# Optimization experiments

Hardware: AMD Instinct MI355X
Metric: run time of the kernel (lower is better)

## Reference

```python
import jax, jax.numpy as jnp
import numpy as np

B, T, E, H, R = 1, 2048, 4096, 16, 64
D = E // H
SCALE_ATTN = float(np.sqrt(D))


def _i8_linear(x, W, b, alpha, beta):
    # W8A8B8O8Linear: int8 in, int8 weight/bias, int8 out with requant epilogue
    acc = jnp.einsum('bte,oe->bto', x.astype(jnp.int32), W.astype(jnp.int32)).astype(jnp.float32)
    y = alpha * acc + beta * b.astype(jnp.float32)
    return jnp.clip(jnp.round(y), -128, 127).astype(jnp.int8)


def _rotate_every_two(x):
    x1, x2 = x[..., ::2], x[..., 1::2]
    return jnp.stack([-x2, x1], axis=-1).reshape(x.shape)


def _sincos(seq_len, dim):
    inv_freq = 1.0 / (10000.0 ** (jnp.arange(0, dim, 2, dtype=jnp.float32) / dim))
    ang = jnp.arange(seq_len, dtype=jnp.float32)[:, None] * inv_freq[None, :]
    return jnp.sin(ang), jnp.cos(ang)


def _apply_rotary(x, sin, cos):
    # duplicate_interleave -> repeat each freq twice along last dim
    sin = jnp.repeat(sin, 2, axis=-1)[None, :, None, :]
    cos = jnp.repeat(cos, 2, axis=-1)[None, :, None, :]
    return x * cos + _rotate_every_two(x) * sin


def setup_inputs():
    key = jax.random.key(0)
    ks = jax.random.split(key, 9)
    i8 = lambda k, s: jax.random.randint(k, s, -128, 128, dtype=jnp.int32).astype(jnp.int8)
    return {
        'hidden_states': i8(ks[0], (B, T, E)),
        'Wq': i8(ks[1], (E, E)), 'bq': i8(ks[2], (E,)),
        'Wk': i8(ks[3], (E, E)), 'bk': i8(ks[4], (E,)),
        'Wv': i8(ks[5], (E, E)), 'bv': i8(ks[6], (E,)),
        'Wo': i8(ks[7], (E, E)),
        'b_out': jax.random.normal(ks[8], (E,), dtype=jnp.float32),
        'alpha_q': 2e-4, 'beta_q': 1.0,
        'alpha_k': 2e-4, 'beta_k': 1.0,
        'alpha_v': 2e-4, 'beta_v': 1.0,
        'alpha_qk': 1e-3, 'alpha_pv': 1e-2, 'alpha_out': 2e-4,
    }


def reference(hidden_states, Wq, bq, Wk, bk, Wv, bv, Wo, b_out,
              alpha_q, beta_q, alpha_k, beta_k, alpha_v, beta_v,
              alpha_qk, alpha_pv, alpha_out):
    # int8 q/k/v projections -> [B, T, H, D]
    q = _i8_linear(hidden_states, Wq, bq, alpha_q, beta_q).reshape(B, T, H, D)
    k = _i8_linear(hidden_states, Wk, bk, alpha_k, beta_k).reshape(B, T, H, D)
    v = _i8_linear(hidden_states, Wv, bv, alpha_v, beta_v).reshape(B, T, H, D)
    v = v.transpose(0, 2, 1, 3)  # [B, H, T, D] int8

    # fused rotary on first R dims (float math on dequantized-per-tensor int8 codes)
    sin, cos = _sincos(T, R)
    qf, kf = q.astype(jnp.float32), k.astype(jnp.float32)
    qf = jnp.concatenate([_apply_rotary(qf[..., :R], sin, cos), qf[..., R:]], axis=-1)
    kf = jnp.concatenate([_apply_rotary(kf[..., :R], sin, cos), kf[..., R:]], axis=-1)
    # torch .to(int8) truncates toward zero
    to_i8 = lambda x: jnp.clip(jnp.trunc(x), -128, 127).astype(jnp.int8)
    q = to_i8(qf.transpose(0, 2, 1, 3))  # [B, H, T, D]
    k = to_i8(kf.transpose(0, 2, 1, 3))

    scores = alpha_qk * jnp.einsum('bhtd,bhsd->bhts', q.astype(jnp.int32), k.astype(jnp.int32)).astype(jnp.float32)
    causal = jnp.tril(jnp.ones((T, T), dtype=bool))
    scores = jnp.where(causal, scores, jnp.finfo(jnp.float32).min)
    probs = jax.nn.softmax(scores / SCALE_ATTN, axis=-1)
    probs = jnp.round(probs * 127.0).astype(jnp.int8)  # requant probs to int8

    acc = jnp.einsum('bhts,bhsd->bhtd', probs.astype(jnp.int32), v.astype(jnp.int32)).astype(jnp.float32)
    attn_out = jnp.clip(jnp.round(alpha_pv * acc), -128, 127).astype(jnp.int8)
    attn_out = attn_out.transpose(0, 2, 1, 3).reshape(B, T, E)  # merge heads

    # W8A8BFP32OFP32Linear
    out = alpha_out * jnp.einsum('bte,oe->bto', attn_out.astype(jnp.int32), Wo.astype(jnp.int32)).astype(jnp.float32) + b_out
    return out
```

## Files before the change

### kernel.cpp

```cpp
#include <hip/hip_runtime.h>
#include <cstdint>
#include <cmath>

#define T_ 2048
#define E_ 4096
#define H_ 16
#define D_ 256
#define NF 32

typedef int v4i  __attribute__((ext_vector_type(4)));

__device__ __forceinline__ int dot4(int a, int b, int c) {
#if __has_builtin(__builtin_amdgcn_sdot4)
  return __builtin_amdgcn_sdot4(a, b, c, false);
#else
  c += ((a << 24) >> 24) * ((b << 24) >> 24);
  c += ((a << 16) >> 24) * ((b << 16) >> 24);
  c += ((a <<  8) >> 24) * ((b <<  8) >> 24);
  c += (a >> 24) * (b >> 24);
  return c;
#endif
}

__device__ __forceinline__ int pack4i(int4 v) {
  return (v.x & 255) | ((v.y & 255) << 8) | ((v.z & 255) << 16) | (v.w << 24);
}

#define GLD_LDS16(g, l)                                                        \
  __builtin_amdgcn_global_load_lds(                                            \
      (const __attribute__((address_space(1))) void*)(g),                      \
      (__attribute__((address_space(3))) void*)(l), 16, 0, 0)

__global__ void sincos_kernel(float* __restrict__ sinT, float* __restrict__ cosT) {
  int idx = blockIdx.x * 256 + threadIdx.x;
  int t = idx >> 5, j = idx & 31;
  float invf = (float)exp(-(double)j * (log(10000.0) / 32.0));
  float ang = (float)t * invf;
  sinT[idx] = (float)sin((double)ang);
  cosT[idx] = (float)cos((double)ang);
}

__global__ __launch_bounds__(256) void repack_kernel(const int* __restrict__ src,
                                                     int8_t* __restrict__ dst) {
  size_t i = (size_t)blockIdx.x * 256 + threadIdx.x;
  const int4* s = (const int4*)src + i * 4;
  int4 a = s[0], b = s[1], c = s[2], d = s[3];
  int4 o;
  o.x = pack4i(a); o.y = pack4i(b); o.z = pack4i(c); o.w = pack4i(d);
  ((int4*)dst)[i] = o;
}

__global__ __launch_bounds__(256) void qkv_gemm_mfma(
    const int8_t* __restrict__ x8,
    const int8_t* __restrict__ Wq8, const int* __restrict__ bq,
    const int8_t* __restrict__ Wk8, const int* __restrict__ bk,
    const int8_t* __restrict__ Wv8, const int* __restrict__ bv,
    const float* __restrict__ alpq, const float* __restrict__ betq,
    const float* __restrict__ alpk, const float* __restrict__ betk,
    const float* __restrict__ alpv, const float* __restrict__ betv,
    int8_t* __restrict__ Q8, int8_t* __restrict__ K8, int8_t* __restrict__ VT)
{
  const int mode = blockIdx.z;
  const int8_t* __restrict__ W = (mode == 0) ? Wq8 : (mode == 1 ? Wk8 : Wv8);
  const int* __restrict__ bs   = (mode == 0) ? bq  : (mode == 1 ? bk  : bv);
  const float alpha = (mode == 0) ? alpq[0] : (mode == 1 ? alpk[0] : alpv[0]);
  const float beta  = (mode == 0) ? betq[0] : (mode == 1 ? betk[0] : betv[0]);

  __shared__ int8_t As[128 * 64];
  __shared__ int8_t Bs[128 * 64];

  const int tid  = threadIdx.x;
  const int wave = tid >> 6, lane = tid & 63;
  const int wm = wave >> 1, wn = wave & 1;
  const int t0 = blockIdx.x * 128, o0 = blockIdx.y * 128;

  const int srow = lane >> 2;
  const int scol = (lane & 3) * 16;
  const int col  = lane & 15;
  const int quad = lane >> 4;

  v4i acc[4][4] = {};

  const int8_t* gA0 = x8 + (size_t)(t0 + wave * 32 + srow) * E_ + scol;
  const int8_t* gB0 = W  + (size_t)(o0 + wave * 32 + srow) * E_ + scol;

  for (int e0 = 0; e0 < E_; e0 += 64) {
    __syncthreads();
    GLD_LDS16(gA0 + e0,                 As + wave * 2048);
    GLD_LDS16(gA0 + e0 + 16 * E_,       As + wave * 2048 + 1024);
    GLD_LDS16(gB0 + e0,                 Bs + wave * 2048);
    GLD_LDS16(gB0 + e0 + 16 * E_,       Bs + wave * 2048 + 1024);
    __syncthreads();

    v4i a[4], b[4];
    #pragma unroll
    for (int i = 0; i < 4; ++i)
      a[i] = *(const v4i*)(As + (wm * 64 + i * 16 + col) * 64 + quad * 16);
    #pragma unroll
    for (int j = 0; j < 4; ++j)
      b[j] = *(const v4i*)(Bs + (wn * 64 + j * 16 + col) * 64 + quad * 16);
    #pragma unroll
    for (int i = 0; i < 4; ++i)
      #pragma unroll
      for (int j = 0; j < 4; ++j)
        acc[i][j] = __builtin_amdgcn_mfma_i32_16x16x64_i8(a[i], b[j], acc[i][j], 0, 0, 0);
  }

  int8_t* __restrict__ dst = (mode == 0) ? Q8 : (mode == 1 ? K8 : VT);
  #pragma unroll
  for (int j = 0; j < 4; ++j) {
    const int o  = o0 + wn * 64 + j * 16 + col;
    const int h  = o >> 8;
    const int dd = o & 255;
    const float bb = (float)bs[o];
    #pragma unroll
    for (int i = 0; i < 4; ++i) {
      const int tb = t0 + wm * 64 + i * 16 + quad * 4;
      int qb[4];
      #pragma unroll
      for (int r = 0; r < 4; ++r) {
        float v = __fadd_rn(__fmul_rn(alpha, (float)acc[i][j][r]),
                            __fmul_rn(beta, bb));
        v = rintf(v);
        v = fminf(fmaxf(v, -128.0f), 127.0f);
        qb[r] = (int)v;
      }
      if (mode == 2) {
        int packed = (qb[0] & 255) | ((qb[1] & 255) << 8) |
                     ((qb[2] & 255) << 16) | ((qb[3] & 255) << 24);
        *(int*)(dst + ((size_t)h * 256 + dd) * T_ + tb) = packed;
      } else {
        #pragma unroll
        for (int r = 0; r < 4; ++r)
          dst[((size_t)h * T_ + tb + r) * D_ + dd] = (int8_t)qb[r];
      }
    }
  }
}

__global__ __launch_bounds__(256) void rope_kernel(
    int8_t* __restrict__ Q8, int8_t* __restrict__ K8,
    const float* __restrict__ sinT, const float* __restrict__ cosT)
{
  int idx = blockIdx.x * 256 + threadIdx.x;
  int c = idx & 3;
  int t = (idx >> 2) & (T_ - 1);
  int h = (idx >> 13) & (H_ - 1);
  int m = idx >> 17;
  int8_t* base = (m == 0 ? Q8 : K8) + ((size_t)h * T_ + t) * D_ + c * 16;
  int4 v = *(int4*)base;
  int u[4] = {v.x, v.y, v.z, v.w};
  const int jb = c * 8;
  #pragma unroll
  for (int ui = 0; ui < 4; ++ui) {
    const int j = jb + ui * 2;
    const float s0 = sinT[t * NF + j],     c0 = cosT[t * NF + j];
    const float s1 = sinT[t * NF + j + 1], c1 = cosT[t * NF + j + 1];
    const int w = u[ui];
    float y0 = (float)((w << 24) >> 24);
    float y1 = (float)((w << 16) >> 24);
    float y2 = (float)((w <<  8) >> 24);
    float y3 = (float)(w >> 24);
    float r0 = __fadd_rn(__fmul_rn(y0, c0), __fmul_rn(-y1, s0));
    float r1 = __fadd_rn(__fmul_rn(y1, c0), __fmul_rn( y0, s0));
    float r2 = __fadd_rn(__fmul_rn(y2, c1), __fmul_rn(-y3, s1));
    float r3 = __fadd_rn(__fmul_rn(y3, c1), __fmul_rn( y2, s1));
    int q0 = (int)fminf(fmaxf(truncf(r0), -128.0f), 127.0f);
    int q1 = (int)fminf(fmaxf(truncf(r1), -128.0f), 127.0f);
    int q2 = (int)fminf(fmaxf(truncf(r2), -128.0f), 127.0f);
    int q3 = (int)fminf(fmaxf(truncf(r3), -128.0f), 127.0f);
    u[ui] = (q0 & 255) | ((q1 & 255) << 8) | ((q2 & 255) << 16) | ((q3 & 255) << 24);
  }
  int4 ov; ov.x = u[0]; ov.y = u[1]; ov.z = u[2]; ov.w = u[3];
  *(int4*)base = ov;
}

__global__ __launch_bounds__(256) void out_gemm_mfma(
    const int8_t* __restrict__ xa, const int8_t* __restrict__ Wo8,
    const float* __restrict__ b_out, const float* __restrict__ p_aout,
    float* __restrict__ out)
{
  const float alpha = p_aout[0];
  __shared__ int8_t As[128 * 64];
  __shared__ int8_t Bs[128 * 64];

  const int tid  = threadIdx.x;
  const int wave = tid >> 6, lane = tid & 63;
  const int wm = wave >> 1, wn = wave & 1;
  const int t0 = blockIdx.x * 128, o0 = blockIdx.y * 128;
  const int srow = lane >> 2, scol = (lane & 3) * 16;
  const int col = lane & 15, quad = lane >> 4;

  v4i acc[4][4] = {};
  const int8_t* gA0 = xa  + (size_t)(t0 + wave * 32 + srow) * E_ + scol;
  const int8_t* gB0 = Wo8 + (size_t)(o0 + wave * 32 + srow) * E_ + scol;

  for (int e0 = 0; e0 < E_; e0 += 64) {
    __syncthreads();
    GLD_LDS16(gA0 + e0,            As + wave * 2048);
    GLD_LDS16(gA0 + e0 + 16 * E_,  As + wave * 2048 + 1024);
    GLD_LDS16(gB0 + e0,            Bs + wave * 2048);
    GLD_LDS16(gB0 + e0 + 16 * E_,  Bs + wave * 2048 + 1024);
    __syncthreads();

    v4i a[4], b[4];
    #pragma unroll
    for (int i = 0; i < 4; ++i)
      a[i] = *(const v4i*)(As + (wm * 64 + i * 16 + col) * 64 + quad * 16);
    #pragma unroll
    for (int j = 0; j < 4; ++j)
      b[j] = *(const v4i*)(Bs + (wn * 64 + j * 16 + col) * 64 + quad * 16);
    #pragma unroll
    for (int i = 0; i < 4; ++i)
      #pragma unroll
      for (int j = 0; j < 4; ++j)
        acc[i][j] = __builtin_amdgcn_mfma_i32_16x16x64_i8(a[i], b[j], acc[i][j], 0, 0, 0);
  }

  #pragma unroll
  for (int j = 0; j < 4; ++j) {
    const int o = o0 + wn * 64 + j * 16 + col;
    const float bb = b_out[o];
    #pragma unroll
    for (int i = 0; i < 4; ++i) {
      #pragma unroll
      for (int r = 0; r < 4; ++r) {
        const int t = t0 + wm * 64 + i * 16 + quad * 4 + r;
        out[(size_t)t * E_ + o] = __fadd_rn(__fmul_rn(alpha, (float)acc[i][j][r]), bb);
      }
    }
  }
}

__global__ __launch_bounds__(256) void attn_ms_chunk(
    const int8_t* __restrict__ Q8, const int8_t* __restrict__ K8,
    const float* __restrict__ p_aqk,
    float* __restrict__ mPart, float* __restrict__ sPart)
{
  const int ch = blockIdx.x;
  const int qi = blockIdx.y;
  const int h  = blockIdx.z;
  if ((ch << 2) > qi) return;

  __shared__ int8_t Qs[4 * 4096];
  __shared__ int8_t KVs[16384];
  __shared__ float  mred[64][2];
  __shared__ float  sred[64][2];

  const int t0  = qi * 64;
  const int tid = threadIdx.x;
  const int wave = tid >> 6, lane = tid & 63;
  const int wm = wave >> 1, wn = wave & 1;
  const int col = lane & 15, quad = lane >> 4;
  const int srow = lane >> 2, scol = (lane & 3) * 16;
  const float aqk = p_aqk[0] * 0.0625f;

  {
    const int8_t* g = Q8 + ((size_t)h * T_ + t0 + wave * 16 + srow) * D_ + scol;
    #pragma unroll
    for (int c = 0; c < 4; ++c)
      GLD_LDS16(g + c * 64, Qs + c * 4096 + wave * 1024);
  }

  const int it0 = ch * 4;
  const int it1 = (it0 + 3 < qi) ? (it0 + 3) : qi;

  float m[8], sm[8];
  #pragma unroll
  for (int u = 0; u < 8; ++u) { m[u] = -INFINITY; sm[u] = 0.0f; }

  for (int it = it0; it <= it1; ++it) {
    const int s0 = it * 64;
    __syncthreads();
    {
      const int8_t* g = K8 + ((size_t)h * T_ + s0 + wave * 16 + srow) * D_ + scol;
      #pragma unroll
      for (int c = 0; c < 4; ++c)
        GLD_LDS16(g + c * 64, KVs + c * 4096 + wave * 1024);
    }
    __syncthreads();
    v4i accS[2][2] = {};
    #pragma unroll
    for (int c = 0; c < 4; ++c) {
      v4i a[2], b[2];
      #pragma unroll
      for (int i = 0; i < 2; ++i)
        a[i] = *(const v4i*)(Qs + c * 4096 + (wm * 32 + i * 16 + col) * 64 + quad * 16);
      #pragma unroll
      for (int j = 0; j < 2; ++j)
        b[j] = *(const v4i*)(KVs + c * 4096 + (wn * 32 + j * 16 + col) * 64 + quad * 16);
      #pragma unroll
      for (int i = 0; i < 2; ++i)
        #pragma unroll
        for (int j = 0; j < 2; ++j)
          accS[i][j] = __builtin_amdgcn_mfma_i32_16x16x64_i8(a[i], b[j], accS[i][j], 0, 0, 0);
    }
    const bool diag = (s0 == t0);
    #pragma unroll
    for (int i = 0; i < 2; ++i) {
      #pragma unroll
      for (int r = 0; r < 4; ++r) {
        const int ri = i * 4 + r;
        const int qrow = t0 + wm * 32 + i * 16 + quad * 4 + r;
        #pragma unroll
        for (int j = 0; j < 2; ++j) {
          const int s = s0 + wn * 32 + j * 16 + col;
          if (!diag || s <= qrow) {
            float l = __fmul_rn(aqk, (float)accS[i][j][r]);
            if (l > m[ri]) { sm[ri] = sm[ri] * expf(m[ri] - l) + 1.0f; m[ri] = l; }
            else           { sm[ri] += expf(l - m[ri]); }
          }
        }
      }
    }
  }

  #pragma unroll
  for (int u = 0; u < 8; ++u) {
    #pragma unroll
    for (int off = 1; off < 16; off <<= 1) {
      float om = __shfl_xor(m[u], off);
      float os = __shfl_xor(sm[u], off);
      float mm = fmaxf(m[u], om);
      float e1 = (m[u] == mm) ? 1.0f : expf(m[u] - mm);
      float e2 = (om   == mm) ? 1.0f : expf(om - mm);
      sm[u] = sm[u] * e1 + os * e2;
      m[u] = mm;
    }
  }
  __syncthreads();
  if (col == 0) {
    #pragma unroll
    for (int u = 0; u < 8; ++u) {
      int row = wm * 32 + (u >> 2) * 16 + quad * 4 + (u & 3);
      mred[row][wn] = m[u];
      sred[row][wn] = sm[u];
    }
  }
  __syncthreads();
  if (col == 0 && wn == 0) {
    #pragma unroll
    for (int u = 0; u < 8; ++u) {
      int row = wm * 32 + (u >> 2) * 16 + quad * 4 + (u & 3);
      float m0 = mred[row][0], m1 = mred[row][1];
      float sa = sred[row][0], sb = sred[row][1];
      float mm = fmaxf(m0, m1);
      float e0 = (m0 == mm) ? 1.0f : expf(m0 - mm);
      float e1 = (m1 == mm) ? 1.0f : expf(m1 - mm);
      size_t base = (((size_t)h * 32 + qi) * 64 + row) * 8 + ch;
      mPart[base] = mm;
      sPart[base] = __fadd_rn(__fmul_rn(sa, e0), __fmul_rn(sb, e1));
    }
  }
}

__global__ __launch_bounds__(256) void attn_ms_combine(
    const float* __restrict__ mPart, const float* __restrict__ sPart,
    float* __restrict__ mFg, float* __restrict__ sFg)
{
  int idx = blockIdx.x * 256 + threadIdx.x;
  int t = idx & (T_ - 1), h = idx >> 11;
  int qi = t >> 6, row = t & 63;
  int nch = (qi >> 2) + 1;
  const float* mp = mPart + (((size_t)h * 32 + qi) * 64 + row) * 8;
  const float* sp = sPart + (((size_t)h * 32 + qi) * 64 + row) * 8;
  float m = mp[0], s = sp[0];
  for (int c = 1; c < nch; ++c) {
    float mc = mp[c], sc = sp[c];
    float mm = fmaxf(m, mc);
    float e1 = (m  == mm) ? 1.0f : expf(m - mm);
    float e2 = (mc == mm) ? 1.0f : expf(mc - mm);
    s = __fadd_rn(__fmul_rn(s, e1), __fmul_rn(sc, e2));
    m = mm;
  }
  mFg[idx] = m;
  sFg[idx] = s;
}

__global__ __launch_bounds__(256) void attn_pv_chunk(
    const int8_t* __restrict__ Q8, const int8_t* __restrict__ K8,
    const int8_t* __restrict__ VT,
    const float* __restrict__ p_aqk,
    const float* __restrict__ mFg, const float* __restrict__ sFg,
    int* __restrict__ P0, int* __restrict__ P1)
{
  const int cc = blockIdx.x;
  const int qi = 31 - blockIdx.y;
  const int h  = blockIdx.z;
  if (cc == 1 && qi < 16) return;

  __shared__ int8_t Qs[4 * 4096];
  __shared__ int8_t KVs[16384];
  __shared__ int8_t Ps[64][64];

  const int t0  = qi * 64;
  const int tid = threadIdx.x;
  const int wave = tid >> 6, lane = tid & 63;
  const int wm = wave >> 1, wn = wave & 1;
  const int col = lane & 15, quad = lane >> 4;
  const int srow = lane >> 2, scol = (lane & 3) * 16;
  const float aqk = p_aqk[0] * 0.0625f;

  {
    const int8_t* g = Q8 + ((size_t)h * T_ + t0 + wave * 16 + srow) * D_ + scol;
    #pragma unroll
    for (int c = 0; c < 4; ++c)
      GLD_LDS16(g + c * 64, Qs + c * 4096 + wave * 1024);
  }

  float mF[8], sF[8];
  #pragma unroll
  for (int u = 0; u < 8; ++u) {
    const int row = wm * 32 + (u >> 2) * 16 + quad * 4 + (u & 3);
    mF[u] = mFg[h * T_ + t0 + row];
    sF[u] = sFg[h * T_ + t0 + row];
  }

  const int it0 = cc * 16;
  const int it1 = (it0 + 15 < qi) ? (it0 + 15) : qi;

  v4i pv[2][8] = {};
  for (int it = it0; it <= it1; ++it) {
    const int s0 = it * 64;
    __syncthreads();
    {
      const int8_t* g = K8 + ((size_t)h * T_ + s0 + wave * 16 + srow) * D_ + scol;
      #pragma unroll
      for (int c = 0; c < 4; ++c)
        GLD_LDS16(g + c * 64, KVs + c * 4096 + wave * 1024);
    }
    __syncthreads();
    v4i accS[2][2] = {};
    #pragma unroll
    for (int c = 0; c < 4; ++c) {
      v4i a[2], b[2];
      #pragma unroll
      for (int i = 0; i < 2; ++i)
        a[i] = *(const v4i*)(Qs + c * 4096 + (wm * 32 + i * 16 + col) * 64 + quad * 16);
      #pragma unroll
      for (int j = 0; j < 2; ++j)
        b[j] = *(const v4i*)(KVs + c * 4096 + (wn * 32 + j * 16 + col) * 64 + quad * 16);
      #pragma unroll
      for (int i = 0; i < 2; ++i)
        #pragma unroll
        for (int j = 0; j < 2; ++j)
          accS[i][j] = __builtin_amdgcn_mfma_i32_16x16x64_i8(a[i], b[j], accS[i][j], 0, 0, 0);
    }
    __syncthreads();
    {
      #pragma unroll
      for (int c = 0; c < 4; ++c) {
        const int drow = (wave * 4 + c) * 16 + srow;
        GLD_LDS16(VT + ((size_t)h * 256 + drow) * T_ + s0 + scol,
                  KVs + (wave * 4 + c) * 1024);
      }
    }
    const bool diag = (s0 == t0);
    #pragma unroll
    for (int i = 0; i < 2; ++i) {
      #pragma unroll
      for (int r = 0; r < 4; ++r) {
        const int ri = i * 4 + r;
        const int qrow = t0 + wm * 32 + i * 16 + quad * 4 + r;
        #pragma unroll
        for (int j = 0; j < 2; ++j) {
          const int s = s0 + wn * 32 + j * 16 + col;
          int q = 0;
          if (!diag || s <= qrow) {
            float l = __fmul_rn(aqk, (float)accS[i][j][r]);
            float p = expf(l - mF[ri]) / sF[ri];
            q = (int)rintf(__fmul_rn(p, 127.0f));
          }
          Ps[wm * 32 + i * 16 + quad * 4 + r][wn * 32 + j * 16 + col] = (int8_t)q;
        }
      }
    }
    __syncthreads();
    v4i a2[2], b2[8];
    #pragma unroll
    for (int i = 0; i < 2; ++i)
      a2[i] = *(const v4i*)&Ps[wm * 32 + i * 16 + col][quad * 16];
    #pragma unroll
    for (int dt = 0; dt < 8; ++dt)
      b2[dt] = *(const v4i*)(KVs + (wn * 128 + dt * 16 + col) * 64 + quad * 16);
    #pragma unroll
    for (int i = 0; i < 2; ++i)
      #pragma unroll
      for (int dt = 0; dt < 8; ++dt)
        pv[i][dt] = __builtin_amdgcn_mfma_i32_16x16x64_i8(a2[i], b2[dt], pv[i][dt], 0, 0, 0);
  }

  int* __restrict__ dst = (cc == 0)
      ? P0 + (((size_t)h * 32 + qi) << 14)
      : P1 + (((size_t)h * 16 + (qi - 16)) << 14);
  #pragma unroll
  for (int i = 0; i < 2; ++i) {
    #pragma unroll
    for (int r = 0; r < 4; ++r) {
      const int trow = wm * 32 + i * 16 + quad * 4 + r;
      #pragma unroll
      for (int dt = 0; dt < 8; ++dt) {
        const int d = wn * 128 + dt * 16 + col;
        dst[trow * 256 + d] = pv[i][dt][r];
      }
    }
  }
}

__global__ __launch_bounds__(256) void attn_pv_combine(
    const int* __restrict__ P0, const int* __restrict__ P1,
    const float* __restrict__ p_apv, int8_t* __restrict__ attn8)
{
  const float apv = p_apv[0];
  int idx = blockIdx.x * 256 + threadIdx.x;
  int d4  = idx & 63;
  int row = (idx >> 6) & 63;
  int qi  = (idx >> 12) & 31;
  int h   = idx >> 17;
  size_t off = (((size_t)h * 32 + qi) << 14) + row * 256 + d4 * 4;
  int4 a = *(const int4*)(P0 + off);
  if (qi >= 16) {
    size_t off1 = (((size_t)h * 16 + (qi - 16)) << 14) + row * 256 + d4 * 4;
    int4 b1 = *(const int4*)(P1 + off1);
    a.x += b1.x; a.y += b1.y; a.z += b1.z; a.w += b1.w;
  }
  int q[4];
  int vv[4] = {a.x, a.y, a.z, a.w};
  #pragma unroll
  for (int r = 0; r < 4; ++r) {
    float y = rintf(__fmul_rn(apv, (float)vv[r]));
    y = fminf(fmaxf(y, -128.0f), 127.0f);
    q[r] = (int)y;
  }
  int packed = (q[0] & 255) | ((q[1] & 255) << 8) | ((q[2] & 255) << 16) | ((q[3] & 255) << 24);
  int t = qi * 64 + row;
  *(int*)(attn8 + (size_t)t * E_ + h * D_ + d4 * 4) = packed;
}

__global__ __launch_bounds__(256) void attn_mfma(
    const int8_t* __restrict__ Q8, const int8_t* __restrict__ K8,
    const int8_t* __restrict__ VT,
    const float* __restrict__ p_aqk, const float* __restrict__ p_apv,
    int8_t* __restrict__ attn8)
{
  __shared__ int8_t Qs[4 * 4096];
  __shared__ int8_t KVs[16384];
  __shared__ int8_t Ps[64][64];
  __shared__ float  mred[64][2];
  __shared__ float  sred[64][2];

  const int h   = blockIdx.y;
  const int t0  = blockIdx.x * 64;
  const int tid = threadIdx.x;
  const int wave = tid >> 6, lane = tid & 63;
  const int wm = wave >> 1, wn = wave & 1;
  const int col = lane & 15, quad = lane >> 4;
  const int srow = lane >> 2, scol = (lane & 3) * 16;
  const float aqk = p_aqk[0] * 0.0625f;
  const float apv = p_apv[0];

  {
    const int8_t* g = Q8 + ((size_t)h * T_ + t0 + wave * 16 + srow) * D_ + scol;
    #pragma unroll
    for (int c = 0; c < 4; ++c)
      GLD_LDS16(g + c * 64, Qs + c * 4096 + wave * 1024);
  }

  const int nt = t0 / 64 + 1;

  float m[8], sm[8];
  #pragma unroll
  for (int u = 0; u < 8; ++u) { m[u] = -INFINITY; sm[u] = 0.0f; }

  for (int it = 0; it < nt; ++it) {
    const int s0 = it * 64;
    __syncthreads();
    {
      const int8_t* g = K8 + ((size_t)h * T_ + s0 + wave * 16 + srow) * D_ + scol;
      #pragma unroll
      for (int c = 0; c < 4; ++c)
        GLD_LDS16(g + c * 64, KVs + c * 4096 + wave * 1024);
    }
    __syncthreads();
    v4i accS[2][2] = {};
    #pragma unroll
    for (int c = 0; c < 4; ++c) {
      v4i a[2], b[2];
      #pragma unroll
      for (int i = 0; i < 2; ++i)
        a[i] = *(const v4i*)(Qs + c * 4096 + (wm * 32 + i * 16 + col) * 64 + quad * 16);
      #pragma unroll
      for (int j = 0; j < 2; ++j)
        b[j] = *(const v4i*)(KVs + c * 4096 + (wn * 32 + j * 16 + col) * 64 + quad * 16);
      #pragma unroll
      for (int i = 0; i < 2; ++i)
        #pragma unroll
        for (int j = 0; j < 2; ++j)
          accS[i][j] = __builtin_amdgcn_mfma_i32_16x16x64_i8(a[i], b[j], accS[i][j], 0, 0, 0);
    }
    const bool diag = (s0 == t0);
    #pragma unroll
    for (int i = 0; i < 2; ++i) {
      #pragma unroll
      for (int r = 0; r < 4; ++r) {
        const int ri = i * 4 + r;
        const int qrow = t0 + wm * 32 + i * 16 + quad * 4 + r;
        #pragma unroll
        for (int j = 0; j < 2; ++j) {
          const int s = s0 + wn * 32 + j * 16 + col;
          if (!diag || s <= qrow) {
            float l = __fmul_rn(aqk, (float)accS[i][j][r]);
            if (l > m[ri]) { sm[ri] = sm[ri] * expf(m[ri] - l) + 1.0f; m[ri] = l; }
            else           { sm[ri] += expf(l - m[ri]); }
          }
        }
      }
    }
  }

  #pragma unroll
  for (int u = 0; u < 8; ++u) {
    #pragma unroll
    for (int off = 1; off < 16; off <<= 1) {
      float om = __shfl_xor(m[u], off);
      float os = __shfl_xor(sm[u], off);
      float mm = fmaxf(m[u], om);
      float e1 = (m[u] == mm) ? 1.0f : expf(m[u] - mm);
      float e2 = (om   == mm) ? 1.0f : expf(om - mm);
      sm[u] = sm[u] * e1 + os * e2;
      m[u] = mm;
    }
  }
  __syncthreads();
  if (col == 0) {
    #pragma unroll
    for (int u = 0; u < 8; ++u) {
      int row = wm * 32 + (u >> 2) * 16 + quad * 4 + (u & 3);
      mred[row][wn] = m[u];
      sred[row][wn] = sm[u];
    }
  }
  __syncthreads();
  float mF[8], sF[8];
  #pragma unroll
  for (int u = 0; u < 8; ++u) {
    int row = wm * 32 + (u >> 2) * 16 + quad * 4 + (u & 3);
    float m0 = mred[row][0], m1 = mred[row][1];
    float sa = sred[row][0], sb = sred[row][1];
    float mm = fmaxf(m0, m1);
    float e0 = (m0 == mm) ? 1.0f : expf(m0 - mm);
    float e1 = (m1 == mm) ? 1.0f : expf(m1 - mm);
    mF[u] = mm;
    sF[u] = __fadd_rn(__fmul_rn(sa, e0), __fmul_rn(sb, e1));
  }

  v4i pv[2][8] = {};
  for (int it = 0; it < nt; ++it) {
    const int s0 = it * 64;
    __syncthreads();
    {
      const int8_t* g = K8 + ((size_t)h * T_ + s0 + wave * 16 + srow) * D_ + scol;
      #pragma unroll
      for (int c = 0; c < 4; ++c)
        GLD_LDS16(g + c * 64, KVs + c * 4096 + wave * 1024);
    }
    __syncthreads();
    v4i accS[2][2] = {};
    #pragma unroll
    for (int c = 0; c < 4; ++c) {
      v4i a[2], b[2];
      #pragma unroll
      for (int i = 0; i < 2; ++i)
        a[i] = *(const v4i*)(Qs + c * 4096 + (wm * 32 + i * 16 + col) * 64 + quad * 16);
      #pragma unroll
      for (int j = 0; j < 2; ++j)
        b[j] = *(const v4i*)(KVs + c * 4096 + (wn * 32 + j * 16 + col) * 64 + quad * 16);
      #pragma unroll
      for (int i = 0; i < 2; ++i)
        #pragma unroll
        for (int j = 0; j < 2; ++j)
          accS[i][j] = __builtin_amdgcn_mfma_i32_16x16x64_i8(a[i], b[j], accS[i][j], 0, 0, 0);
    }
    __syncthreads();
    {
      #pragma unroll
      for (int c = 0; c < 4; ++c) {
        const int drow = (wave * 4 + c) * 16 + srow;
        GLD_LDS16(VT + ((size_t)h * 256 + drow) * T_ + s0 + scol,
                  KVs + (wave * 4 + c) * 1024);
      }
    }
    const bool diag = (s0 == t0);
    #pragma unroll
    for (int i = 0; i < 2; ++i) {
      #pragma unroll
      for (int r = 0; r < 4; ++r) {
        const int ri = i * 4 + r;
        const int qrow = t0 + wm * 32 + i * 16 + quad * 4 + r;
        #pragma unroll
        for (int j = 0; j < 2; ++j) {
          const int s = s0 + wn * 32 + j * 16 + col;
          int q = 0;
          if (!diag || s <= qrow) {
            float l = __fmul_rn(aqk, (float)accS[i][j][r]);
            float p = expf(l - mF[ri]) / sF[ri];
            q = (int)rintf(__fmul_rn(p, 127.0f));
          }
          Ps[wm * 32 + i * 16 + quad * 4 + r][wn * 32 + j * 16 + col] = (int8_t)q;
        }
      }
    }
    __syncthreads();
    v4i a2[2], b2[8];
    #pragma unroll
    for (int i = 0; i < 2; ++i)
      a2[i] = *(const v4i*)&Ps[wm * 32 + i * 16 + col][quad * 16];
    #pragma unroll
    for (int dt = 0; dt < 8; ++dt)
      b2[dt] = *(const v4i*)(KVs + (wn * 128 + dt * 16 + col) * 64 + quad * 16);
    #pragma unroll
    for (int i = 0; i < 2; ++i)
      #pragma unroll
      for (int dt = 0; dt < 8; ++dt)
        pv[i][dt] = __builtin_amdgcn_mfma_i32_16x16x64_i8(a2[i], b2[dt], pv[i][dt], 0, 0, 0);
  }

  #pragma unroll
  for (int i = 0; i < 2; ++i) {
    #pragma unroll
    for (int r = 0; r < 4; ++r) {
      const int t = t0 + wm * 32 + i * 16 + quad * 4 + r;
      #pragma unroll
      for (int dt = 0; dt < 8; ++dt) {
        const int d = wn * 128 + dt * 16 + col;
        float y = rintf(__fmul_rn(apv, (float)pv[i][dt][r]));
        y = fminf(fmaxf(y, -128.0f), 127.0f);
        attn8[(size_t)t * E_ + h * D_ + d] = (int8_t)(int)y;
      }
    }
  }
}

__global__ __launch_bounds__(256) void qkv_gemm_fb(
    const int* __restrict__ xp,
    const int* __restrict__ Wqp, const int* __restrict__ bq,
    const int* __restrict__ Wkp, const int* __restrict__ bk,
    const int* __restrict__ Wvp, const int* __restrict__ bv,
    const float* __restrict__ alpq, const float* __restrict__ betq,
    const float* __restrict__ alpk, const float* __restrict__ betk,
    const float* __restrict__ alpv, const float* __restrict__ betv,
    const float* __restrict__ sinT, const float* __restrict__ cosT,
    int8_t* __restrict__ Q8, int8_t* __restrict__ K8, int8_t* __restrict__ VT)
{
  const int mode = blockIdx.z;
  const int* __restrict__ Wp = (mode == 0) ? Wqp : (mode == 1 ? Wkp : Wvp);
  const int* __restrict__ bs = (mode == 0) ? bq  : (mode == 1 ? bk  : bv);
  const float alpha = (mode == 0) ? alpq[0] : (mode == 1 ? alpk[0] : alpv[0]);
  const float beta  = (mode == 0) ? betq[0] : (mode == 1 ? betk[0] : betv[0]);

  __shared__ int As[64 * 17];
  __shared__ int Bs[64 * 17];
  const int tid = threadIdx.x;
  const int tx = tid & 15, ty = tid >> 4;
  const int t0 = blockIdx.x * 64, o0 = blockIdx.y * 64;
  const int lrow = tid >> 2, lc = tid & 3;
  int acc[4][4] = {};

  for (int e0 = 0; e0 < E_; e0 += 64) {
    const int* xr = xp + (size_t)(t0 + lrow) * E_ + e0 + lc * 16;
    const int* wr = Wp + (size_t)(o0 + lrow) * E_ + e0 + lc * 16;
    int a4[4], b4[4];
    #pragma unroll
    for (int u = 0; u < 4; ++u) a4[u] = pack4i(((const int4*)xr)[u]);
    #pragma unroll
    for (int u = 0; u < 4; ++u) b4[u] = pack4i(((const int4*)wr)[u]);
    __syncthreads();
    int* ap = &As[lrow * 17 + lc * 4];
    ap[0] = a4[0]; ap[1] = a4[1]; ap[2] = a4[2]; ap[3] = a4[3];
    int* bp = &Bs[lrow * 17 + lc * 4];
    bp[0] = b4[0]; bp[1] = b4[1]; bp[2] = b4[2]; bp[3] = b4[3];
    __syncthreads();
    #pragma unroll
    for (int kk = 0; kk < 16; ++kk) {
      int a[4], b[4];
      #pragma unroll
      for (int i = 0; i < 4; ++i) a[i] = As[(ty * 4 + i) * 17 + kk];
      #pragma unroll
      for (int j = 0; j < 4; ++j) b[j] = Bs[(tx * 4 + j) * 17 + kk];
      #pragma unroll
      for (int i = 0; i < 4; ++i)
        #pragma unroll
        for (int j = 0; j < 4; ++j)
          acc[i][j] = dot4(a[i], b[j], acc[i][j]);
    }
  }

  const int ob = o0 + tx * 4;
  const int h  = ob >> 8;
  const int dd = ob & 255;
  #pragma unroll
  for (int i = 0; i < 4; ++i) {
    const int t = t0 + ty * 4 + i;
    float y[4];
    #pragma unroll
    for (int j = 0; j < 4; ++j) {
      float v = __fadd_rn(__fmul_rn(alpha, (float)acc[i][j]),
                          __fmul_rn(beta, (float)bs[ob + j]));
      v = rintf(v);
      y[j] = fminf(fmaxf(v, -128.0f), 127.0f);
    }
    int q0, q1, q2, q3;
    if (mode < 2 && dd < 64) {
      const int j0 = dd >> 1;
      const float s0 = sinT[t * NF + j0],     c0 = cosT[t * NF + j0];
      const float s1 = sinT[t * NF + j0 + 1], c1 = cosT[t * NF + j0 + 1];
      float r0 = __fadd_rn(__fmul_rn(y[0], c0), __fmul_rn(-y[1], s0));
      float r1 = __fadd_rn(__fmul_rn(y[1], c0), __fmul_rn( y[0], s0));
      float r2 = __fadd_rn(__fmul_rn(y[2], c1), __fmul_rn(-y[3], s1));
      float r3 = __fadd_rn(__fmul_rn(y[3], c1), __fmul_rn( y[2], s1));
      q0 = (int)fminf(fmaxf(truncf(r0), -128.0f), 127.0f);
      q1 = (int)fminf(fmaxf(truncf(r1), -128.0f), 127.0f);
      q2 = (int)fminf(fmaxf(truncf(r2), -128.0f), 127.0f);
      q3 = (int)fminf(fmaxf(truncf(r3), -128.0f), 127.0f);
    } else {
      q0 = (int)y[0]; q1 = (int)y[1]; q2 = (int)y[2]; q3 = (int)y[3];
    }
    if (mode == 2) {
      VT[((size_t)h * 256 + dd + 0) * T_ + t] = (int8_t)q0;
      VT[((size_t)h * 256 + dd + 1) * T_ + t] = (int8_t)q1;
      VT[((size_t)h * 256 + dd + 2) * T_ + t] = (int8_t)q2;
      VT[((size_t)h * 256 + dd + 3) * T_ + t] = (int8_t)q3;
    } else {
      int8_t* dst = (mode == 0) ? Q8 : K8;
      int packed = (q0 & 255) | ((q1 & 255) << 8) | ((q2 & 255) << 16) | ((q3 & 255) << 24);
      *(int*)(dst + ((size_t)h * T_ + t) * D_ + dd) = packed;
    }
  }
}

__global__ __launch_bounds__(256) void out_gemm_fb(
    const int8_t* __restrict__ xa, const int* __restrict__ Wop,
    const float* __restrict__ b_out, const float* __restrict__ p_aout,
    float* __restrict__ out)
{
  __shared__ int As[64 * 17];
  __shared__ int Bs[64 * 17];
  const float alpha = p_aout[0];
  const int tid = threadIdx.x;
  const int tx = tid & 15, ty = tid >> 4;
  const int t0 = blockIdx.x * 64, o0 = blockIdx.y * 64;
  const int lrow = tid >> 2, lc = tid & 3;
  int acc[4][4] = {};

  for (int e0 = 0; e0 < E_; e0 += 64) {
    int4 av4 = *(const int4*)(xa + (size_t)(t0 + lrow) * E_ + e0 + lc * 16);
    const int* wr = Wop + (size_t)(o0 + lrow) * E_ + e0 + lc * 16;
    int b4[4];
    #pragma unroll
    for (int u = 0; u < 4; ++u) b4[u] = pack4i(((const int4*)wr)[u]);
    __syncthreads();
    int* ap = &As[lrow * 17 + lc * 4];
    ap[0] = av4.x; ap[1] = av4.y; ap[2] = av4.z; ap[3] = av4.w;
    int* bp = &Bs[lrow * 17 + lc * 4];
    bp[0] = b4[0]; bp[1] = b4[1]; bp[2] = b4[2]; bp[3] = b4[3];
    __syncthreads();
    #pragma unroll
    for (int kk = 0; kk < 16; ++kk) {
      int a[4], b[4];
      #pragma unroll
      for (int i = 0; i < 4; ++i) a[i] = As[(ty * 4 + i) * 17 + kk];
      #pragma unroll
      for (int j = 0; j < 4; ++j) b[j] = Bs[(tx * 4 + j) * 17 + kk];
      #pragma unroll
      for (int i = 0; i < 4; ++i)
        #pragma unroll
        for (int j = 0; j < 4; ++j)
          acc[i][j] = dot4(a[i], b[j], acc[i][j]);
    }
  }
  #pragma unroll
  for (int i = 0; i < 4; ++i) {
    const int t = t0 + ty * 4 + i;
    const int ob = o0 + tx * 4;
    #pragma unroll
    for (int j = 0; j < 4; ++j) {
      out[(size_t)t * E_ + ob + j] =
          __fadd_rn(__fmul_rn(alpha, (float)acc[i][j]), b_out[ob + j]);
    }
  }
}

extern "C" void kernel_launch(void* const* d_in, const int* in_sizes, int n_in,
                              void* d_out, int out_size, void* d_ws, size_t ws_size,
                              hipStream_t stream) {
  const int* hs   = (const int*)d_in[0];
  const int* Wq   = (const int*)d_in[1];
  const int* bq   = (const int*)d_in[2];
  const int* Wk   = (const int*)d_in[3];
  const int* bk   = (const int*)d_in[4];
  const int* Wv   = (const int*)d_in[5];
  const int* bv   = (const int*)d_in[6];
  const int* Wo   = (const int*)d_in[7];
  const float* b_out = (const float*)d_in[8];
  const float* aq   = (const float*)d_in[9];
  const float* btq  = (const float*)d_in[10];
  const float* ak   = (const float*)d_in[11];
  const float* btk  = (const float*)d_in[12];
  const float* av   = (const float*)d_in[13];
  const float* btv  = (const float*)d_in[14];
  const float* aqk  = (const float*)d_in[15];
  const float* apv  = (const float*)d_in[16];
  const float* aout = (const float*)d_in[17];

  const size_t SEG = (size_t)H_ * T_ * D_;
  char* ws = (char*)d_ws;
  int8_t* Q8    = (int8_t*)ws;
  int8_t* K8    = Q8 + SEG;
  int8_t* VT    = K8 + SEG;
  int8_t* attn8 = VT + SEG;
  int8_t* x8    = attn8;
  float*  sinT  = (float*)(ws + 4 * SEG);
  float*  cosT  = sinT + T_ * NF;
  int8_t* Wq8   = (int8_t*)(cosT + T_ * NF);
  int8_t* Wk8   = Wq8 + (size_t)E_ * E_;
  int8_t* Wv8   = Wk8 + (size_t)E_ * E_;
  int8_t* Wo8   = Wv8 + (size_t)E_ * E_;
  const size_t NEED = 4 * SEG + 2 * (size_t)T_ * NF * 4 + 4 * (size_t)E_ * E_;
  const bool big = (ws_size >= NEED);

  sincos_kernel<<<(T_ * NF) / 256, 256, 0, stream>>>(sinT, cosT);

  if (big) {
    repack_kernel<<<(T_ * E_ / 16) / 256, 256, 0, stream>>>(hs, x8);
    repack_kernel<<<(E_ * E_ / 16) / 256, 256, 0, stream>>>(Wq, Wq8);
    repack_kernel<<<(E_ * E_ / 16) / 256, 256, 0, stream>>>(Wk, Wk8);
    repack_kernel<<<(E_ * E_ / 16) / 256, 256, 0, stream>>>(Wv, Wv8);
    repack_kernel<<<(E_ * E_ / 16) / 256, 256, 0, stream>>>(Wo, Wo8);
    qkv_gemm_mfma<<<dim3(T_ / 128, E_ / 128, 3), 256, 0, stream>>>(
        x8, Wq8, bq, Wk8, bk, Wv8, bv, aq, btq, ak, btk, av, btv, Q8, K8, VT);
    rope_kernel<<<(2 * H_ * T_ * 4) / 256, 256, 0, stream>>>(Q8, K8, sinT, cosT);

    int*   P1g   = (int*)Wq8;
    int*   P0g   = (int*)Wk8;
    float* mPart = (float*)attn8;
    float* sPart = mPart + (size_t)H_ * 32 * 64 * 8;
    float* mFg   = sPart + (size_t)H_ * 32 * 64 * 8;
    float* sFg   = mFg + (size_t)H_ * T_;

    attn_ms_chunk<<<dim3(8, 32, H_), 256, 0, stream>>>(Q8, K8, aqk, mPart, sPart);
    attn_ms_combine<<<(H_ * T_) / 256, 256, 0, stream>>>(mPart, sPart, mFg, sFg);
    attn_pv_chunk<<<dim3(2, 32, H_), 256, 0, stream>>>(
        Q8, K8, VT, aqk, mFg, sFg, P0g, P1g);
    attn_pv_combine<<<(H_ * 32 * 64 * 64) / 256, 256, 0, stream>>>(
        P0g, P1g, apv, attn8);

    out_gemm_mfma<<<dim3(T_ / 128, E_ / 128), 256, 0, stream>>>(
        attn8, Wo8, b_out, aout, (float*)d_out);
  } else {
    qkv_gemm_fb<<<dim3(T_ / 64, E_ / 64, 3), 256, 0, stream>>>(
        hs, Wq, bq, Wk, bk, Wv, bv, aq, btq, ak, btk, av, btv,
        sinT, cosT, Q8, K8, VT);
    attn_mfma<<<dim3(T_ / 64, H_), 256, 0, stream>>>(Q8, K8, VT, aqk, apv, attn8);
    out_gemm_fb<<<dim3(T_ / 64, E_ / 64), 256, 0, stream>>>(
        attn8, Wo, b_out, aout, (float*)d_out);
  }
}
```

Before: 701.3 us.

## Triple-buffer LDS with async prefetch and XOR swizzle in QKV/out GEMMs

Both int8 MFMA GEMMs (QKV projection and output projection) switch from a single LDS buffer guarded by two barriers per k-step to a 3-stage ring. Loads are issued two tiles ahead and gated with a vmcnt wait plus one barrier, so global-to-LDS traffic overlaps the MFMA work. The LDS layout also gets an XOR swizzle on the 16-byte column chunks to reduce bank conflicts on the fragment reads, and s_setprio raises wave priority around the MFMA burst. LDS use per block triples to 48KB, which may limit occupancy; the launch bounds now request 3 blocks per SM.

```diff
diff --git a/kernel.cpp b/kernel.cpp
--- a/kernel.cpp
+++ b/kernel.cpp
@@ -50,7 +50,7 @@
   ((int4*)dst)[i] = o;
 }
 
-__global__ __launch_bounds__(256) void qkv_gemm_mfma(
+__global__ __launch_bounds__(256, 3) void qkv_gemm_mfma(
     const int8_t* __restrict__ x8,
     const int8_t* __restrict__ Wq8, const int* __restrict__ bq,
     const int8_t* __restrict__ Wk8, const int* __restrict__ bk,
@@ -66,8 +66,8 @@
   const float alpha = (mode == 0) ? alpq[0] : (mode == 1 ? alpk[0] : alpv[0]);
   const float beta  = (mode == 0) ? betq[0] : (mode == 1 ? betk[0] : betv[0]);
 
-  __shared__ int8_t As[128 * 64];
-  __shared__ int8_t Bs[128 * 64];
+  __shared__ int8_t As[3][8192];
+  __shared__ int8_t Bs[3][8192];
 
   const int tid  = threadIdx.x;
   const int wave = tid >> 6, lane = tid & 63;
@@ -75,7 +75,7 @@
   const int t0 = blockIdx.x * 128, o0 = blockIdx.y * 128;
 
   const int srow = lane >> 2;
-  const int scol = (lane & 3) * 16;
+  const int scol = ((lane & 3) ^ ((lane >> 3) & 3)) * 16;
   const int col  = lane & 15;
   const int quad = lane >> 4;
 
@@ -84,27 +84,52 @@
   const int8_t* gA0 = x8 + (size_t)(t0 + wave * 32 + srow) * E_ + scol;
   const int8_t* gB0 = W  + (size_t)(o0 + wave * 32 + srow) * E_ + scol;
 
-  for (int e0 = 0; e0 < E_; e0 += 64) {
-    __syncthreads();
-    GLD_LDS16(gA0 + e0,                 As + wave * 2048);
-    GLD_LDS16(gA0 + e0 + 16 * E_,       As + wave * 2048 + 1024);
-    GLD_LDS16(gB0 + e0,                 Bs + wave * 2048);
-    GLD_LDS16(gB0 + e0 + 16 * E_,       Bs + wave * 2048 + 1024);
-    __syncthreads();
-
+#define STAGE_QKV(bufi, kt) do {                                               \
+    const int e0_ = (kt) * 64;                                                 \
+    GLD_LDS16(gA0 + e0_,           As[bufi] + wave * 2048);                    \
+    GLD_LDS16(gA0 + e0_ + 16 * E_, As[bufi] + wave * 2048 + 1024);             \
+    GLD_LDS16(gB0 + e0_,           Bs[bufi] + wave * 2048);                    \
+    GLD_LDS16(gB0 + e0_ + 16 * E_, Bs[bufi] + wave * 2048 + 1024);             \
+  } while (0)
+
+  int aoff[4], boff[4];
+  #pragma unroll
+  for (int i = 0; i < 4; ++i) {
+    const int ra = wm * 64 + i * 16 + col;
+    aoff[i] = ra * 64 + ((quad ^ ((ra >> 1) & 3)) * 16);
+    const int rb = wn * 64 + i * 16 + col;
+    boff[i] = rb * 64 + ((quad ^ ((rb >> 1) & 3)) * 16);
+  }
+
+  STAGE_QKV(0, 0);
+  STAGE_QKV(1, 1);
+
+  int cur = 0;
+  for (int kt = 0; kt < 64; ++kt) {
+    if (kt == 63) asm volatile("s_waitcnt vmcnt(0)" ::: "memory");
+    else          asm volatile("s_waitcnt vmcnt(4)" ::: "memory");
+    __builtin_amdgcn_s_barrier();
+    if (kt < 62) {
+      int nb = cur + 2; if (nb >= 3) nb -= 3;
+      STAGE_QKV(nb, kt + 2);
+    }
     v4i a[4], b[4];
     #pragma unroll
     for (int i = 0; i < 4; ++i)
-      a[i] = *(const v4i*)(As + (wm * 64 + i * 16 + col) * 64 + quad * 16);
+      a[i] = *(const v4i*)(As[cur] + aoff[i]);
     #pragma unroll
     for (int j = 0; j < 4; ++j)
-      b[j] = *(const v4i*)(Bs + (wn * 64 + j * 16 + col) * 64 + quad * 16);
+      b[j] = *(const v4i*)(Bs[cur] + boff[j]);
+    __builtin_amdgcn_s_setprio(1);
     #pragma unroll
     for (int i = 0; i < 4; ++i)
       #pragma unroll
       for (int j = 0; j < 4; ++j)
         acc[i][j] = __builtin_amdgcn_mfma_i32_16x16x64_i8(a[i], b[j], acc[i][j], 0, 0, 0);
-  }
+    __builtin_amdgcn_s_setprio(0);
+    cur = (cur == 2) ? 0 : cur + 1;
+  }
+#undef STAGE_QKV
 
   int8_t* __restrict__ dst = (mode == 0) ? Q8 : (mode == 1 ? K8 : VT);
   #pragma unroll
@@ -175,47 +200,73 @@
   *(int4*)base = ov;
 }
 
-__global__ __launch_bounds__(256) void out_gemm_mfma(
+__global__ __launch_bounds__(256, 3) void out_gemm_mfma(
     const int8_t* __restrict__ xa, const int8_t* __restrict__ Wo8,
     const float* __restrict__ b_out, const float* __restrict__ p_aout,
     float* __restrict__ out)
 {
   const float alpha = p_aout[0];
-  __shared__ int8_t As[128 * 64];
-  __shared__ int8_t Bs[128 * 64];
+  __shared__ int8_t As[3][8192];
+  __shared__ int8_t Bs[3][8192];
 
   const int tid  = threadIdx.x;
   const int wave = tid >> 6, lane = tid & 63;
   const int wm = wave >> 1, wn = wave & 1;
   const int t0 = blockIdx.x * 128, o0 = blockIdx.y * 128;
-  const int srow = lane >> 2, scol = (lane & 3) * 16;
+  const int srow = lane >> 2;
+  const int scol = ((lane & 3) ^ ((lane >> 3) & 3)) * 16;
   const int col = lane & 15, quad = lane >> 4;
 
   v4i acc[4][4] = {};
   const int8_t* gA0 = xa  + (size_t)(t0 + wave * 32 + srow) * E_ + scol;
   const int8_t* gB0 = Wo8 + (size_t)(o0 + wave * 32 + srow) * E_ + scol;
 
-  for (int e0 = 0; e0 < E_; e0 += 64) {
-    __syncthreads();
-    GLD_LDS16(gA0 + e0,            As + wave * 2048);
-    GLD_LDS16(gA0 + e0 + 16 * E_,  As + wave * 2048 + 1024);
-    GLD_LDS16(gB0 + e0,            Bs + wave * 2048);
-    GLD_LDS16(gB0 + e0 + 16 * E_,  Bs + wave * 2048 + 1024);
-    __syncthreads();
-
+#define STAGE_OUT(bufi, kt) do {                                               \
+    const int e0_ = (kt) * 64;                                                 \
+    GLD_LDS16(gA0 + e0_,           As[bufi] + wave * 2048);                    \
+    GLD_LDS16(gA0 + e0_ + 16 * E_, As[bufi] + wave * 2048 + 1024);             \
+    GLD_LDS16(gB0 + e0_,           Bs[bufi] + wave * 2048);                    \
+    GLD_LDS16(gB0 + e0_ + 16 * E_, Bs[bufi] + wave * 2048 + 1024);             \
+  } while (0)
+
+  int aoff[4], boff[4];
+  #pragma unroll
+  for (int i = 0; i < 4; ++i) {
+    const int ra = wm * 64 + i * 16 + col;
+    aoff[i] = ra * 64 + ((quad ^ ((ra >> 1) & 3)) * 16);
+    const int rb = wn * 64 + i * 16 + col;
+    boff[i] = rb * 64 + ((quad ^ ((rb >> 1) & 3)) * 16);
+  }
+
+  STAGE_OUT(0, 0);
+  STAGE_OUT(1, 1);
+
+  int cur = 0;
+  for (int kt = 0; kt < 64; ++kt) {
+    if (kt == 63) asm volatile("s_waitcnt vmcnt(0)" ::: "memory");
+    else          asm volatile("s_waitcnt vmcnt(4)" ::: "memory");
+    __builtin_amdgcn_s_barrier();
+    if (kt < 62) {
+      int nb = cur + 2; if (nb >= 3) nb -= 3;
+      STAGE_OUT(nb, kt + 2);
+    }
     v4i a[4], b[4];
     #pragma unroll
     for (int i = 0; i < 4; ++i)
-      a[i] = *(const v4i*)(As + (wm * 64 + i * 16 + col) * 64 + quad * 16);
+      a[i] = *(const v4i*)(As[cur] + aoff[i]);
     #pragma unroll
     for (int j = 0; j < 4; ++j)
-      b[j] = *(const v4i*)(Bs + (wn * 64 + j * 16 + col) * 64 + quad * 16);
+      b[j] = *(const v4i*)(Bs[cur] + boff[j]);
+    __builtin_amdgcn_s_setprio(1);
     #pragma unroll
     for (int i = 0; i < 4; ++i)
       #pragma unroll
       for (int j = 0; j < 4; ++j)
         acc[i][j] = __builtin_amdgcn_mfma_i32_16x16x64_i8(a[i], b[j], acc[i][j], 0, 0, 0);
-  }
+    __builtin_amdgcn_s_setprio(0);
+    cur = (cur == 2) ? 0 : cur + 1;
+  }
+#undef STAGE_OUT
 
   #pragma unroll
   for (int j = 0; j < 4; ++j) {
```

New measurement: 700.8 us. Within noise of the previous version (-0.1%).
